# Optimization experiments

Measured on AMD Instinct MI355X. Metric: run time of the kernel, lower is better.

The kernel has to match this reference:

```python
import jax, jax.numpy as jnp
import numpy as np

B, L, F = 16384, 64, 32
E, A, H = 64, 8, 128


def setup_inputs() -> dict:
    key = jax.random.key(0)
    ks = jax.random.split(key, 16)
    s = 0.1
    return {
        "lane_features": jax.random.normal(ks[0], (B, L, F), jnp.float32),
        "lane_mask": jax.random.randint(ks[1], (B, L), 0, 2).astype(jnp.float32),
        "action_mask": jax.random.randint(ks[2], (B, A), 0, 2).astype(jnp.float32),
        # SingleHeadAttentionPool params (stored [in,out])
        "W": jax.random.normal(ks[3], (F, F), jnp.float32) * s,
        "bW": jnp.zeros((F,), jnp.float32),
        "v": jax.random.normal(ks[4], (F,), jnp.float32) * s,
        "projW": jax.random.normal(ks[5], (F, E), jnp.float32) * s,
        "projb": jnp.zeros((E,), jnp.float32),
        # policy head MLP [E->128->128->A], tanh
        "piW1": jax.random.normal(ks[6], (E, H), jnp.float32) * s,
        "pib1": jnp.zeros((H,), jnp.float32),
        "piW2": jax.random.normal(ks[7], (H, H), jnp.float32) * s,
        "pib2": jnp.zeros((H,), jnp.float32),
        "piW3": jax.random.normal(ks[8], (H, A), jnp.float32) * s,
        "pib3": jnp.zeros((A,), jnp.float32),
        # value head MLP [E->128->128->1], tanh
        "vfW1": jax.random.normal(ks[9], (E, H), jnp.float32) * s,
        "vfb1": jnp.zeros((H,), jnp.float32),
        "vfW2": jax.random.normal(ks[10], (H, H), jnp.float32) * s,
        "vfb2": jnp.zeros((H,), jnp.float32),
        "vfW3": jax.random.normal(ks[11], (H, 1), jnp.float32) * s,
        "vfb3": jnp.zeros((1,), jnp.float32),
    }


def reference(lane_features, lane_mask, action_mask, W, bW, v, projW, projb,
              piW1, pib1, piW2, pib2, piW3, pib3,
              vfW1, vfb1, vfW2, vfb2, vfW3, vfb3):
    X = lane_features                       # [B,L,F]
    mask = lane_mask > 0.5                  # [B,L] bool
    has_active = jnp.any(mask, axis=-1)     # [B]

    # additive attention pool, masked softmax == gather-then-softmax
    Hh = jnp.tanh(jnp.einsum('blf,fg->blg', X, W) + bW)   # [B,L,F]
    scores = jnp.einsum('blf,f->bl', Hh, v)                # [B,L]
    NEG = jnp.float32(-1e30)
    w = jax.nn.softmax(jnp.where(mask, scores, NEG), axis=-1)
    w = jnp.where(mask, w, 0.0)
    pooled = jnp.einsum('bl,blf->bf', w, X)                # [B,F]
    z = pooled @ projW + projb                             # [B,E]
    z = jnp.where(has_active[:, None], z, 0.0)             # empty set -> zeros

    # heads
    h = jnp.tanh(z @ piW1 + pib1)
    h = jnp.tanh(h @ piW2 + pib2)
    logits = h @ piW3 + pib3                               # [B,A]

    g = jnp.tanh(z @ vfW1 + vfb1)
    g = jnp.tanh(g @ vfW2 + vfb2)
    value = (g @ vfW3 + vfb3)[:, 0]                        # [B]

    # hard action masking
    invalid = action_mask <= 0
    masked = jnp.where(invalid, jnp.finfo(logits.dtype).min, logits)
    all_invalid = jnp.all(invalid, axis=1)
    masked = jnp.where(all_invalid[:, None], logits, masked)
    return masked, value
```

## Files before the change

### kernel.cpp

```cpp
#include <hip/hip_runtime.h>
#include <float.h>

#define NBATCH 16384
#define SAFE_MAX 3.3e38f
#define SAFE_NEG -3.3e38f

__device__ __forceinline__ float san(float v) {
    v = (v == v) ? v : 0.0f;
    return fminf(fmaxf(v, SAFE_NEG), SAFE_MAX);
}

__device__ __forceinline__ float tanh_fast(float a) {
    float e = __expf(a + a);
    return fmaf(-2.0f, __builtin_amdgcn_rcpf(e + 1.0f), 1.0f);
}

extern "C" __global__ void __launch_bounds__(256)
pool_kernel(const float* __restrict__ X, const float* __restrict__ LM,
            const float* __restrict__ W, const float* __restrict__ bW,
            const float* __restrict__ vv,
            const float* __restrict__ projW, const float* __restrict__ projb,
            float* __restrict__ zout)
{
    __shared__ float wx[4][64 * 33];
    __shared__ float pooled[4][32];

    const int tid  = threadIdx.x;
    const int w    = __builtin_amdgcn_readfirstlane(tid >> 6);
    const int lane = tid & 63;
    const long b   = (long)blockIdx.x * 4 + w;

    const float4* xp = (const float4*)(X + b * 2048 + lane * 32);
    float x[32];
#pragma unroll
    for (int i = 0; i < 8; ++i) {
        float4 t = xp[i];
        x[4*i+0] = t.x; x[4*i+1] = t.y; x[4*i+2] = t.z; x[4*i+3] = t.w;
    }
    const bool active = LM[b * 64 + lane] > 0.5f;

    float acc[32];
#pragma unroll
    for (int g = 0; g < 32; ++g) acc[g] = 0.0f;
#pragma unroll
    for (int f = 0; f < 32; ++f) {
        const float xf = x[f];
#pragma unroll
        for (int g = 0; g < 32; ++g) acc[g] = fmaf(xf, W[f * 32 + g], acc[g]);
    }
    float score = 0.0f;
#pragma unroll
    for (int g = 0; g < 32; ++g)
        score = fmaf(tanh_fast(acc[g] + bW[g]), vv[g], score);

    float sm = active ? score : -1e30f;
#pragma unroll
    for (int off = 32; off; off >>= 1) sm = fmaxf(sm, __shfl_xor(sm, off));
    float ev = active ? __expf(score - sm) : 0.0f;
    float es = ev;
#pragma unroll
    for (int off = 32; off; off >>= 1) es += __shfl_xor(es, off);
    const float wgt = (es > 0.0f) ? ev * __builtin_amdgcn_rcpf(es) : 0.0f;

#pragma unroll
    for (int i = 0; i < 32; ++i) wx[w][lane * 33 + i] = wgt * x[i];
    __syncthreads();
    {
        const int q = lane >> 5, fr = lane & 31;
        float p = 0.0f;
#pragma unroll
        for (int r = 0; r < 32; ++r) p += wx[w][(q * 32 + r) * 33 + fr];
        p += __shfl_xor(p, 32);
        if (lane < 32) pooled[w][fr] = p;
    }
    __syncthreads();

    float zv = projb[lane];
#pragma unroll
    for (int f = 0; f < 32; ++f)
        zv = fmaf(pooled[w][f], projW[f * 64 + lane], zv);
    const bool any = (__ballot(active) != 0ull);
    zout[b * 64 + lane] = any ? san(zv) : 0.0f;
}

#define ZT 0
#define H1 4160
#define PL 0
extern "C" __global__ void __launch_bounds__(512)
heads_kernel(const float* __restrict__ z, const float* __restrict__ AM,
             const float* __restrict__ piW1, const float* __restrict__ pib1,
             const float* __restrict__ piW2, const float* __restrict__ pib2,
             const float* __restrict__ piW3, const float* __restrict__ pib3,
             const float* __restrict__ vfW1, const float* __restrict__ vfb1,
             const float* __restrict__ vfW2, const float* __restrict__ vfb2,
             const float* __restrict__ vfW3, const float* __restrict__ vfb3,
             float* __restrict__ out)
{
    __shared__ float smem[12352];

    const int tid  = threadIdx.x;
    const int w    = __builtin_amdgcn_readfirstlane(tid >> 6);
    const int el   = tid & 63;
    const bool isPi = (blockIdx.x & 1) == 0;
    const int tile  = blockIdx.x >> 1;

    for (int i = tid; i < 4096; i += 512)
        smem[ZT + (i >> 6) * 65 + (i & 63)] = z[(long)tile * 4096 + i];
    __syncthreads();

    const float* W1 = isPi ? piW1 : vfW1;
    const float* b1 = isPi ? pib1 : vfb1;
    const float* W2 = isPi ? piW2 : vfW2;
    const float* b2 = isPi ? pib2 : vfb2;

    float acc[16];
#pragma unroll
    for (int i = 0; i < 16; ++i) acc[i] = b1[w * 16 + i];
#pragma unroll 8
    for (int e = 0; e < 64; ++e) {
        const float zv = smem[ZT + el * 65 + e];
        const float* wr = W1 + e * 128 + w * 16;
#pragma unroll
        for (int i = 0; i < 16; ++i) acc[i] = fmaf(zv, wr[i], acc[i]);
    }
#pragma unroll
    for (int i = 0; i < 16; ++i)
        smem[H1 + (w * 16 + i) * 64 + el] = tanh_fast(acc[i]);
    __syncthreads();

    float a2[16];
#pragma unroll
    for (int i = 0; i < 16; ++i) a2[i] = b2[w * 16 + i];
#pragma unroll 8
    for (int j = 0; j < 128; ++j) {
        const float hv = smem[H1 + j * 64 + el];
        const float* wr = W2 + j * 128 + w * 16;
#pragma unroll
        for (int i = 0; i < 16; ++i) a2[i] = fmaf(hv, wr[i], a2[i]);
    }

    if (isPi) {
        float pl[8];
#pragma unroll
        for (int a = 0; a < 8; ++a) pl[a] = 0.0f;
#pragma unroll
        for (int i = 0; i < 16; ++i) {
            const float h2 = tanh_fast(a2[i]);
            const float* wr = piW3 + (w * 16 + i) * 8;
#pragma unroll
            for (int a = 0; a < 8; ++a) pl[a] = fmaf(h2, wr[a], pl[a]);
        }
#pragma unroll
        for (int a = 0; a < 8; ++a)
            smem[PL + w * 512 + el * 8 + a] = pl[a];
        __syncthreads();

        const int rel = tid >> 3, ra = tid & 7;
        float lg = pib3[ra];
#pragma unroll
        for (int w2 = 0; w2 < 8; ++w2)
            lg += smem[PL + w2 * 512 + rel * 8 + ra];
        lg = san(lg);
        const long rb = (long)tile * 64 + rel;
        const float am = AM[rb * 8 + ra];
        const bool inv = (am <= 0.0f);
        const unsigned long long bal = __ballot(inv);
        const int grp = (tid & 63) >> 3;
        const bool allinv = (((bal >> (grp * 8)) & 0xFFull) == 0xFFull);
        out[rb * 8 + ra] = allinv ? lg : (inv ? SAFE_NEG : lg);
    } else {
        float pv = 0.0f;
#pragma unroll
        for (int i = 0; i < 16; ++i)
            pv = fmaf(tanh_fast(a2[i]), vfW3[w * 16 + i], pv);
        smem[PL + el * 8 + w] = pv;
        __syncthreads();

        if (tid < 64) {
            float val = vfb3[0];
#pragma unroll
            for (int w2 = 0; w2 < 8; ++w2) val += smem[PL + tid * 8 + w2];
            out[(long)NBATCH * 8 + (long)tile * 64 + tid] = san(val);
        }
    }
}

#define LZ    0
#define LH1f  4096
#define LPLf  12288
#define LWX   4096
#define LPOOL 12800
#define WXS   17

extern "C" __global__ void __launch_bounds__(512, 2)
fused_kernel(const float* __restrict__ X, const float* __restrict__ LM,
             const float* __restrict__ AM,
             const float* __restrict__ W, const float* __restrict__ bW,
             const float* __restrict__ vv,
             const float* __restrict__ projW, const float* __restrict__ projb,
             const float* __restrict__ piW1, const float* __restrict__ pib1,
             const float* __restrict__ piW2, const float* __restrict__ pib2,
             const float* __restrict__ piW3, const float* __restrict__ pib3,
             const float* __restrict__ vfW1, const float* __restrict__ vfb1,
             const float* __restrict__ vfW2, const float* __restrict__ vfb2,
             const float* __restrict__ vfW3, const float* __restrict__ vfb3,
             float* __restrict__ out)
{
    __shared__ float smem[16384];

    const int tid  = threadIdx.x;
    const int w    = __builtin_amdgcn_readfirstlane(tid >> 6);
    const int lane = tid & 63;

    float4 xv[8];
    float  mval;
    {
        const long b0 = (long)blockIdx.x * 64 + w;
        const float4* xp = (const float4*)(X + b0 * 2048 + lane * 32);
#pragma unroll
        for (int i = 0; i < 8; ++i) xv[i] = xp[i];
        mval = LM[b0 * 64 + lane];
    }

#pragma unroll 1
    for (int it = 0; it < 8; ++it) {
        const int eL = it * 8 + w;
        float4 xn[8];
        float  mn = 0.0f;
        if (it < 7) {
            const long bn = (long)blockIdx.x * 64 + (it + 1) * 8 + w;
            const float4* xp = (const float4*)(X + bn * 2048 + lane * 32);
#pragma unroll
            for (int i = 0; i < 8; ++i) xn[i] = xp[i];
            mn = LM[bn * 64 + lane];
        }
        float x[32];
#pragma unroll
        for (int i = 0; i < 8; ++i) {
            x[4*i+0] = xv[i].x; x[4*i+1] = xv[i].y;
            x[4*i+2] = xv[i].z; x[4*i+3] = xv[i].w;
        }
        float acc[32];
#pragma unroll
        for (int g = 0; g < 32; ++g) acc[g] = 0.0f;
#pragma unroll
        for (int f = 0; f < 32; ++f) {
            const float xf = x[f];
#pragma unroll
            for (int g = 0; g < 32; ++g) acc[g] = fmaf(xf, W[f * 32 + g], acc[g]);
        }
        float score = 0.0f;
#pragma unroll
        for (int g = 0; g < 32; ++g)
            score = fmaf(tanh_fast(acc[g] + bW[g]), vv[g], score);

        const bool active = mval > 0.5f;
        float sm = active ? score : -1e30f;
#pragma unroll
        for (int off = 32; off; off >>= 1) sm = fmaxf(sm, __shfl_xor(sm, off));
        float ev = active ? __expf(score - sm) : 0.0f;
        float es = ev;
#pragma unroll
        for (int off = 32; off; off >>= 1) es += __shfl_xor(es, off);
        const float wgt = (es > 0.0f) ? (ev / es) : 0.0f;

        float* wxp = &smem[LWX + w * (64 * WXS)];
#pragma unroll 1
        for (int P = 0; P < 2; ++P) {
            __syncthreads();
#pragma unroll
            for (int fr = 0; fr < 16; ++fr)
                wxp[lane * WXS + fr] = wgt * x[P * 16 + fr];
            __syncthreads();
            const int q = lane >> 4, fr = lane & 15;
            float p = 0.0f;
#pragma unroll
            for (int r = 0; r < 16; ++r) p += wxp[(q * 16 + r) * WXS + fr];
            p += __shfl_xor(p, 16);
            p += __shfl_xor(p, 32);
            if (lane < 16) smem[LPOOL + w * 32 + P * 16 + fr] = p;
        }
        __syncthreads();

        float zv = projb[lane];
#pragma unroll
        for (int f = 0; f < 32; ++f)
            zv = fmaf(smem[LPOOL + w * 32 + f], projW[f * 64 + lane], zv);
        const bool any = (__ballot(active) != 0ull);
        zv = any ? zv : 0.0f;
        smem[LZ + lane * 64 + eL] = san(zv);

        if (it < 7) {
#pragma unroll
            for (int i = 0; i < 8; ++i) xv[i] = xn[i];
            mval = mn;
        }
    }
    __syncthreads();

    const int el = lane;
    {
        float acc[16];
#pragma unroll
        for (int i = 0; i < 16; ++i) acc[i] = pib1[w * 16 + i];
#pragma unroll 8
        for (int e = 0; e < 64; ++e) {
            const float zv = smem[LZ + e * 64 + el];
            const float* wr = piW1 + e * 128 + w * 16;
#pragma unroll
            for (int i = 0; i < 16; ++i) acc[i] = fmaf(zv, wr[i], acc[i]);
        }
#pragma unroll
        for (int i = 0; i < 16; ++i)
            smem[LH1f + (w * 16 + i) * 64 + el] = tanh_fast(acc[i]);
        __syncthreads();

        float a2[16];
#pragma unroll
        for (int i = 0; i < 16; ++i) a2[i] = pib2[w * 16 + i];
#pragma unroll 8
        for (int j = 0; j < 128; ++j) {
            const float hv = smem[LH1f + j * 64 + el];
            const float* wr = piW2 + j * 128 + w * 16;
#pragma unroll
            for (int i = 0; i < 16; ++i) a2[i] = fmaf(hv, wr[i], a2[i]);
        }
        float pl[8];
#pragma unroll
        for (int a = 0; a < 8; ++a) pl[a] = 0.0f;
#pragma unroll
        for (int i = 0; i < 16; ++i) {
            const float h2 = tanh_fast(a2[i]);
            const float* wr = piW3 + (w * 16 + i) * 8;
#pragma unroll
            for (int a = 0; a < 8; ++a) pl[a] = fmaf(h2, wr[a], pl[a]);
        }
#pragma unroll
        for (int a = 0; a < 8; ++a)
            smem[LPLf + w * 512 + el * 8 + a] = pl[a];
        __syncthreads();

        const int rel = tid >> 3, ra = tid & 7;
        float lg = pib3[ra];
#pragma unroll
        for (int w2 = 0; w2 < 8; ++w2)
            lg += smem[LPLf + w2 * 512 + rel * 8 + ra];
        lg = san(lg);
        const long rb = (long)blockIdx.x * 64 + rel;
        const float am = AM[rb * 8 + ra];
        const bool inv = (am <= 0.0f);
        const unsigned long long bal = __ballot(inv);
        const int grp = (tid & 63) >> 3;
        const bool allinv = (((bal >> (grp * 8)) & 0xFFull) == 0xFFull);
        out[rb * 8 + ra] = allinv ? lg : (inv ? SAFE_NEG : lg);
        __syncthreads();
    }
    {
        float acc[16];
#pragma unroll
        for (int i = 0; i < 16; ++i) acc[i] = vfb1[w * 16 + i];
#pragma unroll 8
        for (int e = 0; e < 64; ++e) {
            const float zv = smem[LZ + e * 64 + el];
            const float* wr = vfW1 + e * 128 + w * 16;
#pragma unroll
            for (int i = 0; i < 16; ++i) acc[i] = fmaf(zv, wr[i], acc[i]);
        }
#pragma unroll
        for (int i = 0; i < 16; ++i)
            smem[LH1f + (w * 16 + i) * 64 + el] = tanh_fast(acc[i]);
        __syncthreads();

        float a2[16];
#pragma unroll
        for (int i = 0; i < 16; ++i) a2[i] = vfb2[w * 16 + i];
#pragma unroll 8
        for (int j = 0; j < 128; ++j) {
            const float hv = smem[LH1f + j * 64 + el];
            const float* wr = vfW2 + j * 128 + w * 16;
#pragma unroll
            for (int i = 0; i < 16; ++i) a2[i] = fmaf(hv, wr[i], a2[i]);
        }
        float pv = 0.0f;
#pragma unroll
        for (int i = 0; i < 16; ++i)
            pv = fmaf(tanh_fast(a2[i]), vfW3[w * 16 + i], pv);
        smem[LPLf + el * 8 + w] = pv;
        __syncthreads();

        if (tid < 64) {
            float val = vfb3[0];
#pragma unroll
            for (int w2 = 0; w2 < 8; ++w2) val += smem[LPLf + tid * 8 + w2];
            out[(long)NBATCH * 8 + (long)blockIdx.x * 64 + tid] = san(val);
        }
    }
}

extern "C" void kernel_launch(void* const* d_in, const int* in_sizes, int n_in,
                              void* d_out, int out_size, void* d_ws, size_t ws_size,
                              hipStream_t stream) {
    const float* X     = (const float*)d_in[0];
    const float* LM    = (const float*)d_in[1];
    const float* AM    = (const float*)d_in[2];
    const float* W     = (const float*)d_in[3];
    const float* bW    = (const float*)d_in[4];
    const float* vv    = (const float*)d_in[5];
    const float* projW = (const float*)d_in[6];
    const float* projb = (const float*)d_in[7];
    const float* piW1  = (const float*)d_in[8];
    const float* pib1  = (const float*)d_in[9];
    const float* piW2  = (const float*)d_in[10];
    const float* pib2  = (const float*)d_in[11];
    const float* piW3  = (const float*)d_in[12];
    const float* pib3  = (const float*)d_in[13];
    const float* vfW1  = (const float*)d_in[14];
    const float* vfb1  = (const float*)d_in[15];
    const float* vfW2  = (const float*)d_in[16];
    const float* vfb2  = (const float*)d_in[17];
    const float* vfW3  = (const float*)d_in[18];
    const float* vfb3  = (const float*)d_in[19];

    float* outp = (float*)d_out;
    const size_t zbytes = (size_t)NBATCH * 64 * sizeof(float);

    if (ws_size >= zbytes) {
        float* z = (float*)d_ws;
        pool_kernel<<<NBATCH / 4, 256, 0, stream>>>(
            X, LM, W, bW, vv, projW, projb, z);
        heads_kernel<<<(NBATCH / 64) * 2, 512, 0, stream>>>(
            z, AM, piW1, pib1, piW2, pib2, piW3, pib3,
            vfW1, vfb1, vfW2, vfb2, vfW3, vfb3, outp);
    } else {
        fused_kernel<<<NBATCH / 64, 512, 0, stream>>>(
            X, LM, AM, W, bW, vv, projW, projb,
            piW1, pib1, piW2, pib2, piW3, pib3,
            vfW1, vfb1, vfW2, vfb2, vfW3, vfb3, outp);
    }
}
```

Baseline: 264.9 us.

## Compute pool_kernel attention scores with bf16 MFMA instead of scalar FMAs

Rewrites pool_kernel so the X·W projection for the attention scores runs on 16x16x32 bf16 MFMA instructions. W is transposed into LDS as bf16, and X is truncated to bf16 fragments in registers. Scores are reduced with lane shuffles and the weighted pooling is done with shuffles rather than a padded LDS transpose. This cuts scalar FMA work and LDS traffic, but lowers score precision to bf16 and adds extra syncs. The file also contains a fused_kernel, so this path may not be the one that gets launched.

```diff
diff --git a/kernel.cpp b/kernel.cpp
--- a/kernel.cpp
+++ b/kernel.cpp
@@ -5,6 +5,9 @@
 #define SAFE_MAX 3.3e38f
 #define SAFE_NEG -3.3e38f
 
+typedef __attribute__((ext_vector_type(8))) short bf16x8;
+typedef __attribute__((ext_vector_type(4))) float f32x4;
+
 __device__ __forceinline__ float san(float v) {
     v = (v == v) ? v : 0.0f;
     return fminf(fmaxf(v, SAFE_NEG), SAFE_MAX);
@@ -15,70 +18,125 @@
     return fmaf(-2.0f, __builtin_amdgcn_rcpf(e + 1.0f), 1.0f);
 }
 
-extern "C" __global__ void __launch_bounds__(256)
+__device__ __forceinline__ unsigned short f2bf_rne(float v) {
+    unsigned int u = __float_as_uint(v);
+    return (unsigned short)((u + 0x7FFFu + ((u >> 16) & 1u)) >> 16);
+}
+
+extern "C" __global__ void __launch_bounds__(256, 4)
 pool_kernel(const float* __restrict__ X, const float* __restrict__ LM,
             const float* __restrict__ W, const float* __restrict__ bW,
             const float* __restrict__ vv,
             const float* __restrict__ projW, const float* __restrict__ projb,
             float* __restrict__ zout)
 {
-    __shared__ float wx[4][64 * 33];
-    __shared__ float pooled[4][32];
+    __shared__ __align__(16) short wt[32 * 40];
+    __shared__ float sc[4][64];
+    __shared__ float mk[4][64];
+    __shared__ float pool_s[4][32];
 
     const int tid  = threadIdx.x;
     const int w    = __builtin_amdgcn_readfirstlane(tid >> 6);
     const int lane = tid & 63;
+    const int c    = lane & 15;
+    const int quad = lane >> 4;
     const long b   = (long)blockIdx.x * 4 + w;
 
-    const float4* xp = (const float4*)(X + b * 2048 + lane * 32);
-    float x[32];
-#pragma unroll
-    for (int i = 0; i < 8; ++i) {
-        float4 t = xp[i];
-        x[4*i+0] = t.x; x[4*i+1] = t.y; x[4*i+2] = t.z; x[4*i+3] = t.w;
-    }
-    const bool active = LM[b * 64 + lane] > 0.5f;
-
-    float acc[32];
-#pragma unroll
-    for (int g = 0; g < 32; ++g) acc[g] = 0.0f;
-#pragma unroll
-    for (int f = 0; f < 32; ++f) {
-        const float xf = x[f];
-#pragma unroll
-        for (int g = 0; g < 32; ++g) acc[g] = fmaf(xf, W[f * 32 + g], acc[g]);
-    }
-    float score = 0.0f;
-#pragma unroll
-    for (int g = 0; g < 32; ++g)
-        score = fmaf(tanh_fast(acc[g] + bW[g]), vv[g], score);
-
-    float sm = active ? score : -1e30f;
-#pragma unroll
-    for (int off = 32; off; off >>= 1) sm = fmaxf(sm, __shfl_xor(sm, off));
-    float ev = active ? __expf(score - sm) : 0.0f;
+    for (int i = tid; i < 1024; i += 256) {
+        const int n = i >> 5, k = i & 31;
+        wt[n * 40 + k] = (short)f2bf_rne(W[k * 32 + n]);
+    }
+
+    float xr[4][8];
+#pragma unroll
+    for (int t = 0; t < 4; ++t) {
+        const float4* p = (const float4*)(X + b * 2048 + (16 * t + c) * 32 + quad * 8);
+        float4 a0 = p[0], a1 = p[1];
+        xr[t][0] = a0.x; xr[t][1] = a0.y; xr[t][2] = a0.z; xr[t][3] = a0.w;
+        xr[t][4] = a1.x; xr[t][5] = a1.y; xr[t][6] = a1.z; xr[t][7] = a1.w;
+    }
+    const float ml = LM[b * 64 + lane];
+    const bool active = ml > 0.5f;
+
+    union { bf16x8 v; unsigned int u[4]; } afr[4];
+#pragma unroll
+    for (int t = 0; t < 4; ++t)
+#pragma unroll
+        for (int j2 = 0; j2 < 4; ++j2)
+            afr[t].u[j2] = __builtin_amdgcn_perm(
+                __float_as_uint(xr[t][2 * j2 + 1]),
+                __float_as_uint(xr[t][2 * j2]), 0x07060302u);
+
+    __syncthreads();
+
+    union { bf16x8 v; uint4 q; } bfr[2];
+#pragma unroll
+    for (int u = 0; u < 2; ++u)
+        bfr[u].q = *((const uint4*)&wt[(16 * u + c) * 40 + quad * 8]);
+
+    f32x4 acc[4][2];
+#pragma unroll
+    for (int t = 0; t < 4; ++t)
+#pragma unroll
+        for (int u = 0; u < 2; ++u) {
+            acc[t][u] = (f32x4){0.f, 0.f, 0.f, 0.f};
+            acc[t][u] = __builtin_amdgcn_mfma_f32_16x16x32_bf16(
+                afr[t].v, bfr[u].v, acc[t][u], 0, 0, 0);
+        }
+
+    const float bw0 = bW[c], bw1 = bW[16 + c];
+    const float vv0 = vv[c], vv1 = vv[16 + c];
+    mk[w][lane] = ml;
+#pragma unroll
+    for (int t = 0; t < 4; ++t)
+#pragma unroll
+        for (int r = 0; r < 4; ++r) {
+            float s = tanh_fast(acc[t][0][r] + bw0) * vv0
+                    + tanh_fast(acc[t][1][r] + bw1) * vv1;
+            s += __shfl_xor(s, 1);
+            s += __shfl_xor(s, 2);
+            s += __shfl_xor(s, 4);
+            s += __shfl_xor(s, 8);
+            if (c == t * 4 + r)
+                sc[w][16 * t + quad * 4 + r] = s;
+        }
+    __syncthreads();
+
+    const float s0 = sc[w][lane];
+    float smx = active ? s0 : -1e30f;
+#pragma unroll
+    for (int off = 32; off; off >>= 1) smx = fmaxf(smx, __shfl_xor(smx, off));
+    float ev = active ? __expf(s0 - smx) : 0.0f;
     float es = ev;
 #pragma unroll
     for (int off = 32; off; off >>= 1) es += __shfl_xor(es, off);
-    const float wgt = (es > 0.0f) ? ev * __builtin_amdgcn_rcpf(es) : 0.0f;
-
-#pragma unroll
-    for (int i = 0; i < 32; ++i) wx[w][lane * 33 + i] = wgt * x[i];
-    __syncthreads();
-    {
-        const int q = lane >> 5, fr = lane & 31;
-        float p = 0.0f;
-#pragma unroll
-        for (int r = 0; r < 32; ++r) p += wx[w][(q * 32 + r) * 33 + fr];
-        p += __shfl_xor(p, 32);
-        if (lane < 32) pooled[w][fr] = p;
+    const float rcpS = __builtin_amdgcn_rcpf(es);
+
+    float wgt[4];
+#pragma unroll
+    for (int t = 0; t < 4; ++t) {
+        const float sr = sc[w][16 * t + c];
+        const float mr = mk[w][16 * t + c];
+        wgt[t] = (mr > 0.5f && es > 0.0f) ? __expf(sr - smx) * rcpS : 0.0f;
+    }
+
+#pragma unroll
+    for (int j = 0; j < 8; ++j) {
+        float p = wgt[0] * xr[0][j];
+#pragma unroll
+        for (int t = 1; t < 4; ++t) p = fmaf(wgt[t], xr[t][j], p);
+        p += __shfl_xor(p, 1);
+        p += __shfl_xor(p, 2);
+        p += __shfl_xor(p, 4);
+        p += __shfl_xor(p, 8);
+        if (c == 0) pool_s[w][quad * 8 + j] = p;
     }
     __syncthreads();
 
     float zv = projb[lane];
 #pragma unroll
     for (int f = 0; f < 32; ++f)
-        zv = fmaf(pooled[w][f], projW[f * 64 + lane], zv);
+        zv = fmaf(pool_s[w][f], projW[f * 64 + lane], zv);
     const bool any = (__ballot(active) != 0ull);
     zout[b * 64 + lane] = any ? san(zv) : 0.0f;
 }
@@ -207,7 +265,6 @@
              float* __restrict__ out)
 {
     __shared__ float smem[16384];
-
     const int tid  = threadIdx.x;
     const int w    = __builtin_amdgcn_readfirstlane(tid >> 6);
     const int lane = tid & 63;
@@ -221,7 +278,6 @@
         for (int i = 0; i < 8; ++i) xv[i] = xp[i];
         mval = LM[b0 * 64 + lane];
     }
-
 #pragma unroll 1
     for (int it = 0; it < 8; ++it) {
         const int eL = it * 8 + w;
@@ -289,7 +345,6 @@
         const bool any = (__ballot(active) != 0ull);
         zv = any ? zv : 0.0f;
         smem[LZ + lane * 64 + eL] = san(zv);
-
         if (it < 7) {
 #pragma unroll
             for (int i = 0; i < 8; ++i) xv[i] = xn[i];
```

Result: faster. 257.8 us (-2.7%).
